# Kernel tuning notes

Hardware: AMD Instinct MI355X
Metric: run time of the kernel (lower is better)

The kernel has to match this reference:

```python
import jax, jax.numpy as jnp
import numpy as np

DIM = 1024
HEADS = 16
HEAD_DIM = DIM // HEADS
WINDOW = 128


def setup_inputs() -> dict:
    key = jax.random.key(0)
    k1, k2, k3, k4 = jax.random.split(key, 4)
    B, T = 2, 2048
    x = jax.random.normal(k1, (B, T, DIM), dtype=jnp.float32)
    # nn.Linear(dim, 3*dim, bias=False): weight [3*dim, dim]; y = x @ W.T
    W_qkv = jax.random.normal(k2, (3 * DIM, DIM), dtype=jnp.float32) * (1.0 / np.sqrt(DIM))
    W_proj = jax.random.normal(k3, (DIM, DIM), dtype=jnp.float32) * (1.0 / np.sqrt(DIM))
    b_proj = jax.random.normal(k4, (DIM,), dtype=jnp.float32) * 0.01
    return {"x": x, "W_qkv": W_qkv, "W_proj": W_proj, "b_proj": b_proj}


def reference(x, W_qkv, W_proj, b_proj) -> jnp.ndarray:
    B, T, C = x.shape
    scale = HEAD_DIM ** -0.5
    qkv = jnp.einsum('btc,oc->bto', x, W_qkv)  # [B,T,3*D]
    qkv = qkv.reshape(B, T, 3, HEADS, HEAD_DIM)
    qkv = jnp.transpose(qkv, (2, 0, 3, 1, 4))  # [3,B,H,T,hd]
    q, k, v = qkv[0], qkv[1], qkv[2]
    # sliding-window mask: attend iff |i-j| <= WINDOW
    idx = jnp.arange(T)
    mask = jnp.abs(idx[:, None] - idx[None, :]) <= WINDOW  # [T,T]
    scores = jnp.einsum('bhqd,bhkd->bhqk', q, k) * scale  # [B,H,T,T]
    scores = jnp.where(mask[None, None], scores, jnp.finfo(scores.dtype).min)
    attn = jax.nn.softmax(scores, axis=-1)
    out = jnp.einsum('bhqk,bhkd->bhqd', attn, v)  # [B,H,T,hd]
    out = jnp.transpose(out, (0, 2, 1, 3)).reshape(B, T, C)
    return jnp.einsum('btc,oc->bto', out, W_proj) + b_proj
```

## Files before the change

### kernel.cpp

```cpp
#include <hip/hip_runtime.h>
#include <hip/hip_bf16.h>
#include <cstdint>
#include <cstddef>

#define DIMC 1024
#define HEADS 16
#define HD 64
#define WINDOW 128
#define BB 2
#define TT 2048
#define NTOK (BB*TT)
#define QKVN (3*DIMC)

typedef __bf16 bf16;
typedef __bf16 bf16x8 __attribute__((ext_vector_type(8)));
typedef __bf16 bf16x4 __attribute__((ext_vector_type(4)));
typedef float f32x4 __attribute__((ext_vector_type(4)));
typedef unsigned int u32;

typedef const __attribute__((address_space(1))) u32* gp1_t;
typedef __attribute__((address_space(3))) u32* lp3_t;

__device__ __forceinline__ void gload16(const void* g, void* l) {
  __builtin_amdgcn_global_load_lds((gp1_t)g, (lp3_t)l, 16, 0, 0);
}

__device__ __forceinline__ u32 lds_u32(const void* p) {
  return (u32)(uintptr_t)(__attribute__((address_space(3))) const void*)p;
}

__device__ __forceinline__ void BAR() {
  asm volatile("" ::: "memory");
  __builtin_amdgcn_s_barrier();
  asm volatile("" ::: "memory");
}

__global__ void cast3_kernel(const float* __restrict__ x,
                             const float* __restrict__ wq,
                             const float* __restrict__ wp,
                             bf16* __restrict__ xo,
                             bf16* __restrict__ wqo,
                             bf16* __restrict__ wpo) {
  const int NX = NTOK * DIMC / 4;
  const int NQ = QKVN * DIMC / 4;
  const int NP = DIMC * DIMC / 4;
  const int total = NX + NQ + NP;
  typedef float float4v __attribute__((ext_vector_type(4)));
  for (int i = blockIdx.x * blockDim.x + threadIdx.x; i < total;
       i += gridDim.x * blockDim.x) {
    const float4v* src; bf16* dst; int j;
    if (i < NX)            { src = (const float4v*)x;  dst = xo;  j = i; }
    else if (i < NX + NQ)  { src = (const float4v*)wq; dst = wqo; j = i - NX; }
    else                   { src = (const float4v*)wp; dst = wpo; j = i - NX - NQ; }
    float4v v = src[j];
    bf16x4 o;
    o[0] = (bf16)v[0]; o[1] = (bf16)v[1]; o[2] = (bf16)v[2]; o[3] = (bf16)v[3];
    ((bf16x4*)dst)[j] = o;
  }
}

__device__ __forceinline__ bf16x8 lds_frag(const bf16* base, int row, int colb) {
  const char* p = (const char*)base + row * 128 + (colb ^ ((row & 7) << 4));
  return *(const bf16x8*)p;
}

template<int BN, int N_, bool BF16OUT>
__global__ __launch_bounds__(256, 2) void gemm_kernel(
    const bf16* __restrict__ A, const bf16* __restrict__ Bw,
    bf16* __restrict__ Cb, float* __restrict__ Cf,
    const float* __restrict__ bias) {
  constexpr int NT = 16;
  constexpr int NB = BN / 32;
  constexpr int LPT = 4 + BN / 32;
  __shared__ bf16 Al[2][128 * 64];
  __shared__ bf16 Bl[2][BN * 64];

  const int tid = threadIdx.x;
  const int w = tid >> 6, l = tid & 63;
  const int wm = w >> 1, wn = w & 1;
  const int lr = l & 15, lg = l >> 4;

  const int nwg = gridDim.x;
  const int bid = blockIdx.x;
  const int wg = (bid & 7) * (nwg >> 3) + (bid >> 3);
  const int bm = wg & 31;
  const int bn = wg >> 5;

  const char* Ag = (const char*)A + (size_t)(bm * 128) * 2048;
  const char* Bg = (const char*)Bw + (size_t)(bn * BN) * 2048;

  auto stageA = [&](bf16* lds, int kt) {
#pragma unroll
    for (int i = 0; i < 4; i++) {
      const int R0 = w * 32 + i * 8;
      const int r = R0 + (l >> 3);
      const char* src = Ag + (size_t)r * 2048 + kt * 128
                        + (((l & 7) * 16) ^ ((r & 7) << 4));
      gload16(src, lds + R0 * 64);
    }
  };
  auto stageB = [&](bf16* lds, int kt) {
#pragma unroll
    for (int i = 0; i < NB; i++) {
      const int R0 = w * (BN / 4) + i * 8;
      const int r = R0 + (l >> 3);
      const char* src = Bg + (size_t)r * 2048 + kt * 128
                        + (((l & 7) * 16) ^ ((r & 7) << 4));
      gload16(src, lds + R0 * 64);
    }
  };

  stageA(Al[0], 0); stageB(Bl[0], 0);
  stageA(Al[1], 1); stageB(Bl[1], 1);
  if constexpr (LPT == 7) asm volatile("s_waitcnt vmcnt(7)" ::: "memory");
  else                    asm volatile("s_waitcnt vmcnt(8)" ::: "memory");
  BAR();

  f32x4 acc[4][NB] = {};

  for (int kt = 0; kt < NT; ++kt) {
    const bf16* Ac = Al[kt & 1];
    const bf16* Bc = Bl[kt & 1];

    bf16x8 af[4][2], bf[NB][2];
#pragma unroll
    for (int m = 0; m < 4; m++)
#pragma unroll
      for (int kk = 0; kk < 2; kk++)
        af[m][kk] = lds_frag(Ac, wm * 64 + m * 16 + lr, kk * 64 + lg * 16);
#pragma unroll
    for (int n = 0; n < NB; n++)
#pragma unroll
      for (int kk = 0; kk < 2; kk++)
        bf[n][kk] = lds_frag(Bc, wn * (BN / 2) + n * 16 + lr, kk * 64 + lg * 16);

    asm volatile("s_waitcnt lgkmcnt(0)" ::: "memory");
    __builtin_amdgcn_sched_barrier(0);
    BAR();

    if (kt + 2 < NT) {
      stageA(Al[kt & 1], kt + 2);
      stageB(Bl[kt & 1], kt + 2);
    }

    __builtin_amdgcn_s_setprio(1);
#pragma unroll
    for (int kk = 0; kk < 2; kk++)
#pragma unroll
      for (int m = 0; m < 4; m++)
#pragma unroll
        for (int n = 0; n < NB; n++)
          acc[m][n] = __builtin_amdgcn_mfma_f32_16x16x32_bf16(
              af[m][kk], bf[n][kk], acc[m][n], 0, 0, 0);
    __builtin_amdgcn_s_setprio(0);

    if (kt < NT - 2) {
      if constexpr (LPT == 7) asm volatile("s_waitcnt vmcnt(7)" ::: "memory");
      else                    asm volatile("s_waitcnt vmcnt(8)" ::: "memory");
    } else {
      asm volatile("s_waitcnt vmcnt(0)" ::: "memory");
    }
    BAR();
  }

#pragma unroll
  for (int m = 0; m < 4; m++) {
    const int row = bm * 128 + wm * 64 + m * 16 + lg * 4;
#pragma unroll
    for (int n = 0; n < NB; n++) {
      const int col = bn * BN + wn * (BN / 2) + n * 16 + lr;
#pragma unroll
      for (int j = 0; j < 4; j++) {
        if constexpr (BF16OUT)
          Cb[(size_t)(row + j) * N_ + col] = (bf16)acc[m][n][j];
        else
          Cf[(size_t)(row + j) * N_ + col] = acc[m][n][j] + bias[col];
      }
    }
  }
}

__global__ __launch_bounds__(256, 2) void attn_kernel(const bf16* __restrict__ qkv,
                                                      bf16* __restrict__ out) {
  __shared__ bf16 Kl[3][64 * 64];
  __shared__ bf16 Vl[3][64 * 64];

  const int tid = threadIdx.x, w = tid >> 6, l = tid & 63;
  const int qb = blockIdx.x & 15, bh = blockIdx.x >> 4;
  const int b = bh >> 4, h = bh & 15;
  const int q0 = qb * 128;
  const int lr = l & 15, lg = l >> 4;
  const float SC = 0.18033688011f;

  const char* qkv_b = (const char*)qkv + (size_t)(b * TT) * (QKVN * 2);

  size_t koff[2]; u32 kdst[2];
#pragma unroll
  for (int i = 0; i < 2; i++) {
    const int R0 = 8 * (w + 4 * i);
    const int r = R0 + (l >> 3);
    const int colb = (((l & 7) * 16) ^ (((l >> 3) & 7) << 4));
    koff[i] = (size_t)r * (QKVN * 2) + (DIMC + h * HD) * 2 + colb;
    kdst[i] = (u32)(R0 * 64);
  }
  size_t voff[2]; u32 vdst[2];
#pragma unroll
  for (int i = 0; i < 2; i++) {
    const int c = tid + 256 * i;
    const int t = c >> 3, w_ = c & 7;
    const int kv = (t & 15) * 4 + (w_ >> 1);
    const int d  = (t >> 4) * 16 + (w_ & 1) * 8;
    voff[i] = (size_t)kv * (QKVN * 2) + (2 * DIMC + h * HD + d) * 2;
    vdst[i] = (u32)((w + 4 * i) * 512);
  }

  auto stage = [&](int buf, int kb) {
    const char* rowb = qkv_b + (size_t)(kb * 64) * (QKVN * 2);
#pragma unroll
    for (int i = 0; i < 2; i++)
      gload16(rowb + koff[i], &Kl[buf][kdst[i]]);
#pragma unroll
    for (int i = 0; i < 2; i++)
      gload16(rowb + voff[i], &Vl[buf][vdst[i]]);
  };

  bf16x8 qf[2][2];
#pragma unroll
  for (int qi = 0; qi < 2; qi++) {
    const bf16* qp = qkv + (size_t)(b * TT + q0 + w * 32 + qi * 16 + lr) * QKVN
                     + h * HD + lg * 8;
    qf[qi][0] = *(const bf16x8*)qp;
    qf[qi][1] = *(const bf16x8*)(qp + 32);
  }

  f32x4 Oa[2][4] = {};
  float mrow[2] = {-1e30f, -1e30f}, lrow[2] = {0.f, 0.f};

  int kb0 = 2 * qb - 2; if (kb0 < 0) kb0 = 0;
  int kb1 = 2 * qb + 3; if (kb1 > 31) kb1 = 31;

  stage(0, kb0);
  stage(1, kb0 + 1);
  asm volatile("s_waitcnt vmcnt(4)" ::: "memory");
  BAR();

  for (int kb = kb0; kb <= kb1; ++kb) {
    const int c = (kb - kb0) % 3;
    if (kb + 2 <= kb1) stage((c + 2) % 3, kb + 2);

    const bf16* Kb = &Kl[c][0];
    f32x4 Sa[2][4] = {};
#pragma unroll
    for (int kf = 0; kf < 2; kf++)
#pragma unroll
      for (int nf = 0; nf < 4; nf++) {
        const char* kp = (const char*)Kb + (nf * 16 + lr) * 128
                         + ((kf * 64 + lg * 16) ^ ((lr & 7) << 4));
        bf16x8 kfr = *(const bf16x8*)kp;
        Sa[0][nf] = __builtin_amdgcn_mfma_f32_16x16x32_bf16(kfr, qf[0][kf], Sa[0][nf], 0, 0, 0);
        Sa[1][nf] = __builtin_amdgcn_mfma_f32_16x16x32_bf16(kfr, qf[1][kf], Sa[1][nf], 0, 0, 0);
      }

    bf16x4 tr0[4][2], tr1[4][2];
    {
      const u32 vbase = lds_u32(&Vl[c][0]) + l * 8;
#pragma unroll
      for (int nf = 0; nf < 4; nf++)
#pragma unroll
        for (int kf = 0; kf < 2; kf++) {
          const u32 a = vbase + (u32)((nf * 16 + kf * 8) * 128);
          asm volatile("ds_read_b64_tr_b16 %0, %1"
                       : "=v"(tr0[nf][kf]) : "v"(a));
          asm volatile("ds_read_b64_tr_b16 %0, %1 offset:512"
                       : "=v"(tr1[nf][kf]) : "v"(a));
        }
    }

    const int kvb = kb * 64;
    float scl[2];
    bf16x8 pa[2][2];
#pragma unroll
    for (int qi = 0; qi < 2; qi++) {
      const int qrow = q0 + w * 32 + qi * 16 + lr;
      float mblk = -1e30f;
#pragma unroll
      for (int nf = 0; nf < 4; nf++)
#pragma unroll
        for (int j = 0; j < 4; j++) {
          int kv = kvb + nf * 16 + lg * 4 + j;
          int dq = qrow - kv;
          float s = Sa[qi][nf][j] * SC;
          if (dq > WINDOW || dq < -WINDOW) s = -1e30f;
          Sa[qi][nf][j] = s;
          mblk = fmaxf(mblk, s);
        }
      mblk = fmaxf(mblk, __shfl_xor(mblk, 16));
      mblk = fmaxf(mblk, __shfl_xor(mblk, 32));

      float mn = fmaxf(mrow[qi], mblk);
      scl[qi] = exp2f(mrow[qi] - mn);
      mrow[qi] = mn;

      float rsum = 0.f;
#pragma unroll
      for (int nf = 0; nf < 4; nf++)
#pragma unroll
        for (int j = 0; j < 4; j++) {
          float e = exp2f(Sa[qi][nf][j] - mn);
          Sa[qi][nf][j] = e;
          rsum += e;
        }
      rsum += __shfl_xor(rsum, 16);
      rsum += __shfl_xor(rsum, 32);
      lrow[qi] = lrow[qi] * scl[qi] + rsum;

#pragma unroll
      for (int kf = 0; kf < 2; kf++)
#pragma unroll
        for (int e = 0; e < 4; e++) {
          pa[qi][kf][e]     = (bf16)Sa[qi][2 * kf][e];
          pa[qi][kf][e + 4] = (bf16)Sa[qi][2 * kf + 1][e];
        }

#pragma unroll
      for (int j = 0; j < 4; j++) {
        float so = __shfl(scl[qi], lg * 4 + j);
#pragma unroll
        for (int nf = 0; nf < 4; nf++) Oa[qi][nf][j] *= so;
      }
    }

    asm volatile("s_waitcnt lgkmcnt(0)" ::: "memory");
    __builtin_amdgcn_sched_barrier(0);
#pragma unroll
    for (int nf = 0; nf < 4; nf++)
#pragma unroll
      for (int kf = 0; kf < 2; kf++) {
        bf16x8 vb;
#pragma unroll
        for (int e = 0; e < 4; e++) {
          vb[e]     = tr0[nf][kf][e];
          vb[e + 4] = tr1[nf][kf][e];
        }
        Oa[0][nf] = __builtin_amdgcn_mfma_f32_16x16x32_bf16(pa[0][kf], vb, Oa[0][nf], 0, 0, 0);
        Oa[1][nf] = __builtin_amdgcn_mfma_f32_16x16x32_bf16(pa[1][kf], vb, Oa[1][nf], 0, 0, 0);
      }

    if (kb < kb1) {
      if (kb + 2 <= kb1) asm volatile("s_waitcnt vmcnt(4)" ::: "memory");
      else               asm volatile("s_waitcnt vmcnt(0)" ::: "memory");
    }
    BAR();
  }

#pragma unroll
  for (int qi = 0; qi < 2; qi++) {
    float lo[4];
#pragma unroll
    for (int j = 0; j < 4; j++) lo[j] = __shfl(lrow[qi], lg * 4 + j);
#pragma unroll
    for (int nf = 0; nf < 4; nf++) {
#pragma unroll
      for (int j = 0; j < 4; j++) {
        int q = q0 + w * 32 + qi * 16 + lg * 4 + j;
        int d = nf * 16 + lr;
        out[(size_t)(b * TT + q) * DIMC + h * HD + d] = (bf16)(Oa[qi][nf][j] / lo[j]);
      }
    }
  }
}

extern "C" void kernel_launch(void* const* d_in, const int* in_sizes, int n_in,
                              void* d_out, int out_size, void* d_ws, size_t ws_size,
                              hipStream_t stream) {
  const float* x     = (const float*)d_in[0];
  const float* Wqkv  = (const float*)d_in[1];
  const float* Wproj = (const float*)d_in[2];
  const float* bproj = (const float*)d_in[3];
  float* out = (float*)d_out;

  char* ws = (char*)d_ws;
  bf16* xb   = (bf16*)(ws);
  bf16* wqb  = (bf16*)(ws + 8388608);
  bf16* wpb  = (bf16*)(ws + 14680064);
  bf16* qkvb = (bf16*)(ws + 16777216);
  bf16* aob  = (bf16*)(ws + 41943040);

  cast3_kernel<<<2048, 256, 0, stream>>>(x, Wqkv, Wproj, xb, wqb, wpb);
  gemm_kernel<96, QKVN, true><<<1024, 256, 0, stream>>>(xb, wqb, qkvb, nullptr, nullptr);
  attn_kernel<<<512, 256, 0, stream>>>(qkvb, aob);
  gemm_kernel<128, DIMC, false><<<256, 256, 0, stream>>>(aob, wpb, nullptr, out, bproj);
}
```

Before: 90.04 us.

## Use 128x128 tiles for QKV GEMM with XCD-aware 8x8 block grouping

The QKV projection GEMM now uses 128x128 output tiles instead of 128x96, so it launches 768 workgroups instead of 1024, and each tile does more MFMA work per LDS load. Block indices are remapped so that each group of eight consecutive blocks covers an 8x(N/2) region of tiles, meant to improve L2 reuse of A and B rows per XCD. The wait counts are simplified to a uniform vmcnt(8). The larger accumulator tile raises register pressure, and the wave count changes relative to the CU count.

```diff
diff --git a/kernel.cpp b/kernel.cpp
--- a/kernel.cpp
+++ b/kernel.cpp
@@ -64,83 +64,70 @@
   return *(const bf16x8*)p;
 }
 
-template<int BN, int N_, bool BF16OUT>
+template<int N_, bool BF16OUT>
 __global__ __launch_bounds__(256, 2) void gemm_kernel(
     const bf16* __restrict__ A, const bf16* __restrict__ Bw,
     bf16* __restrict__ Cb, float* __restrict__ Cf,
     const float* __restrict__ bias) {
   constexpr int NT = 16;
-  constexpr int NB = BN / 32;
-  constexpr int LPT = 4 + BN / 32;
+  constexpr int Nb = N_ / 128;
   __shared__ bf16 Al[2][128 * 64];
-  __shared__ bf16 Bl[2][BN * 64];
+  __shared__ bf16 Bl[2][128 * 64];
 
   const int tid = threadIdx.x;
   const int w = tid >> 6, l = tid & 63;
   const int wm = w >> 1, wn = w & 1;
   const int lr = l & 15, lg = l >> 4;
 
-  const int nwg = gridDim.x;
   const int bid = blockIdx.x;
-  const int wg = (bid & 7) * (nwg >> 3) + (bid >> 3);
-  const int bm = wg & 31;
-  const int bn = wg >> 5;
+  const int x = bid & 7, i = bid >> 3;
+  const int bm = 8 * (x >> 1) + (i & 7);
+  const int bn = (Nb / 2) * (x & 1) + (i >> 3);
 
   const char* Ag = (const char*)A + (size_t)(bm * 128) * 2048;
-  const char* Bg = (const char*)Bw + (size_t)(bn * BN) * 2048;
-
-  auto stageA = [&](bf16* lds, int kt) {
-#pragma unroll
-    for (int i = 0; i < 4; i++) {
-      const int R0 = w * 32 + i * 8;
+  const char* Bg = (const char*)Bw + (size_t)(bn * 128) * 2048;
+
+  auto stageT = [&](bf16* lds, const char* gbase, int kt) {
+#pragma unroll
+    for (int i2 = 0; i2 < 4; i2++) {
+      const int R0 = w * 32 + i2 * 8;
       const int r = R0 + (l >> 3);
-      const char* src = Ag + (size_t)r * 2048 + kt * 128
+      const char* src = gbase + (size_t)r * 2048 + kt * 128
                         + (((l & 7) * 16) ^ ((r & 7) << 4));
       gload16(src, lds + R0 * 64);
     }
   };
-  auto stageB = [&](bf16* lds, int kt) {
-#pragma unroll
-    for (int i = 0; i < NB; i++) {
-      const int R0 = w * (BN / 4) + i * 8;
-      const int r = R0 + (l >> 3);
-      const char* src = Bg + (size_t)r * 2048 + kt * 128
-                        + (((l & 7) * 16) ^ ((r & 7) << 4));
-      gload16(src, lds + R0 * 64);
-    }
-  };
-
-  stageA(Al[0], 0); stageB(Bl[0], 0);
-  stageA(Al[1], 1); stageB(Bl[1], 1);
-  if constexpr (LPT == 7) asm volatile("s_waitcnt vmcnt(7)" ::: "memory");
-  else                    asm volatile("s_waitcnt vmcnt(8)" ::: "memory");
+
+  stageT(Al[0], Ag, 0); stageT(Bl[0], Bg, 0);
+  stageT(Al[1], Ag, 1); stageT(Bl[1], Bg, 1);
+  asm volatile("s_waitcnt vmcnt(8)" ::: "memory");
   BAR();
 
-  f32x4 acc[4][NB] = {};
+  f32x4 acc[4][4] = {};
 
   for (int kt = 0; kt < NT; ++kt) {
     const bf16* Ac = Al[kt & 1];
     const bf16* Bc = Bl[kt & 1];
 
-    bf16x8 af[4][2], bf[NB][2];
+    bf16x8 af[4][2], bf[4][2];
 #pragma unroll
     for (int m = 0; m < 4; m++)
 #pragma unroll
       for (int kk = 0; kk < 2; kk++)
         af[m][kk] = lds_frag(Ac, wm * 64 + m * 16 + lr, kk * 64 + lg * 16);
 #pragma unroll
-    for (int n = 0; n < NB; n++)
+    for (int n = 0; n < 4; n++)
 #pragma unroll
       for (int kk = 0; kk < 2; kk++)
-        bf[n][kk] = lds_frag(Bc, wn * (BN / 2) + n * 16 + lr, kk * 64 + lg * 16);
+        bf[n][kk] = lds_frag(Bc, wn * 64 + n * 16 + lr, kk * 64 + lg * 16);
 
     asm volatile("s_waitcnt lgkmcnt(0)" ::: "memory");
     __builtin_amdgcn_sched_barrier(0);
     BAR();
 
     if (kt + 2 < NT) {
-      stageA(Al[kt & 1], kt + 2);
-      stageB(Bl[kt & 1], kt + 2);
+      stageT(Al[kt & 1], Ag, kt + 2);
+      stageT(Bl[kt & 1], Bg, kt + 2);
     }
 
     __builtin_amdgcn_s_setprio(1);
@@ -149,17 +136,13 @@
 #pragma unroll
       for (int m = 0; m < 4; m++)
 #pragma unroll
-        for (int n = 0; n < NB; n++)
+        for (int n = 0; n < 4; n++)
           acc[m][n] = __builtin_amdgcn_mfma_f32_16x16x32_bf16(
               af[m][kk], bf[n][kk], acc[m][n], 0, 0, 0);
     __builtin_amdgcn_s_setprio(0);
 
-    if (kt < NT - 2) {
-      if constexpr (LPT == 7) asm volatile("s_waitcnt vmcnt(7)" ::: "memory");
-      else                    asm volatile("s_waitcnt vmcnt(8)" ::: "memory");
-    } else {
-      asm volatile("s_waitcnt vmcnt(0)" ::: "memory");
-    }
+    if (kt < NT - 2) asm volatile("s_waitcnt vmcnt(8)" ::: "memory");
+    else             asm volatile("s_waitcnt vmcnt(0)" ::: "memory");
     BAR();
   }
 
@@ -167,8 +150,8 @@
   for (int m = 0; m < 4; m++) {
     const int row = bm * 128 + wm * 64 + m * 16 + lg * 4;
 #pragma unroll
-    for (int n = 0; n < NB; n++) {
-      const int col = bn * BN + wn * (BN / 2) + n * 16 + lr;
+    for (int n = 0; n < 4; n++) {
+      const int col = bn * 128 + wn * 64 + n * 16 + lr;
 #pragma unroll
       for (int j = 0; j < 4; j++) {
         if constexpr (BF16OUT)
@@ -387,7 +370,7 @@
   bf16* aob  = (bf16*)(ws + 41943040);
 
   cast3_kernel<<<2048, 256, 0, stream>>>(x, Wqkv, Wproj, xb, wqb, wpb);
-  gemm_kernel<96, QKVN, true><<<1024, 256, 0, stream>>>(xb, wqb, qkvb, nullptr, nullptr);
+  gemm_kernel<QKVN, true><<<768, 256, 0, stream>>>(xb, wqb, qkvb, nullptr, nullptr);
   attn_kernel<<<512, 256, 0, stream>>>(qkvb, aob);
-  gemm_kernel<128, DIMC, false><<<256, 256, 0, stream>>>(aob, wpb, nullptr, out, bproj);
-}
+  gemm_kernel<DIMC, false><<<256, 256, 0, stream>>>(aob, wpb, nullptr, out, bproj);
+}
```

New measurement: 84.32 us. 6.4% less time.
